# Optimization experiments

Hardware: AMD Instinct MI355X
Metric: run time of the kernel (lower is better)

## Reference

```python
import jax, jax.numpy as jnp
import numpy as np

HIDDEN = 768
HEADS = 12
HEAD_DIM = HIDDEN // HEADS


def setup_inputs() -> dict:
    key = jax.random.key(0)
    ks = jax.random.split(key, 6)
    B, N = 32, 577  # N = 1 CLS + 576 patches
    x = jax.random.normal(ks[0], (B, N, HIDDEN), dtype=jnp.float32)
    seg_bias = jax.random.uniform(ks[1], (B, N - 1), dtype=jnp.float32)
    w_qkv = jax.random.normal(ks[2], (HIDDEN, 3 * HIDDEN), dtype=jnp.float32) * 0.02
    b_qkv = jnp.zeros((3 * HIDDEN,), dtype=jnp.float32)
    w_proj = jax.random.normal(ks[3], (HIDDEN, HIDDEN), dtype=jnp.float32) * 0.02
    b_proj = jnp.zeros((HIDDEN,), dtype=jnp.float32)
    seg_scale = jnp.ones((), dtype=jnp.float32)
    return {"x": x, "seg_bias": seg_bias, "w_qkv": w_qkv, "b_qkv": b_qkv,
            "w_proj": w_proj, "b_proj": b_proj, "seg_scale": seg_scale}


def reference(x, seg_bias, w_qkv, b_qkv, w_proj, b_proj, seg_scale):
    B, N, _ = x.shape
    scale = HEAD_DIM ** -0.5
    qkv = x @ w_qkv + b_qkv                       # (B, N, 3*H*D)
    qkv = qkv.reshape(B, N, 3, HEADS, HEAD_DIM)
    q = qkv[:, :, 0].transpose(0, 2, 1, 3)        # (B, H, N, D)
    k = qkv[:, :, 1].transpose(0, 2, 1, 3)
    v = qkv[:, :, 2].transpose(0, 2, 1, 3)
    attn = jnp.einsum('bhqd,bhkd->bhqk', q, k) * scale  # (B, H, N, N)
    # additive seg bias on CLS-query row, patch keys only (cols 1:)
    bias = (seg_bias * seg_scale)[:, None, None, :]     # (B,1,1,N-1)
    attn = attn.at[:, :, 0:1, 1:].add(bias)
    attn = jax.nn.softmax(attn, axis=-1)
    out = jnp.einsum('bhqk,bhkd->bhqd', attn, v)        # (B, H, N, D)
    out = out.transpose(0, 2, 1, 3).reshape(B, N, HIDDEN)
    return out @ w_proj + b_proj
```

## Files before the change

### kernel.cpp

```cpp
#include <hip/hip_runtime.h>


typedef unsigned short bf16_t;
typedef __attribute__((ext_vector_type(8))) short short8;
typedef __attribute__((ext_vector_type(4))) short short4v;
typedef __attribute__((ext_vector_type(4))) float f32x4;

#define B_    32
#define N_    577
#define BN_   18464
#define HID_  768
#define NH_   12
#define HD_   64
#define QKVC_ 2304
#define NPAD_ 640
#define PB_LD 68

__device__ __forceinline__ bf16_t f2bf(float f) {
  union { float f; unsigned u; } x; x.f = f;
  unsigned r = x.u + 0x7fffu + ((x.u >> 16) & 1u);
  return (bf16_t)(r >> 16);
}

__device__ __forceinline__ unsigned cvt_pk_bf16(float a, float b) {
  unsigned r;
  asm("v_cvt_pk_bf16_f32 %0, %1, %2" : "=v"(r) : "v"(a), "v"(b));
  return r;
}

__global__ __launch_bounds__(256) void cast_kernel(const float* __restrict__ in,
                                                   bf16_t* __restrict__ out, int n4) {
  int i = blockIdx.x * 256 + threadIdx.x;
  if (i >= n4) return;
  float4 v = ((const float4*)in)[i];
  ushort4 o;
  o.x = f2bf(v.x); o.y = f2bf(v.y); o.z = f2bf(v.z); o.w = f2bf(v.w);
  ((ushort4*)out)[i] = o;
}

__global__ __launch_bounds__(256) void transpose_cast_kernel(const float* __restrict__ in,
                                                             bf16_t* __restrict__ out,
                                                             int R, int C) {
  __shared__ float tile[32][33];
  int c0 = blockIdx.x * 32, r0 = blockIdx.y * 32;
  int tx = threadIdx.x, ty = threadIdx.y;
  #pragma unroll
  for (int i = ty; i < 32; i += 8)
    tile[i][tx] = in[(size_t)(r0 + i) * C + c0 + tx];
  __syncthreads();
  #pragma unroll
  for (int i = ty; i < 32; i += 8)
    out[(size_t)(c0 + i) * R + r0 + tx] = f2bf(tile[tx][i]);
}

__device__ __forceinline__ void stage256(const bf16_t* __restrict__ A,
                                         const bf16_t* __restrict__ Bt,
                                         int M, int m0, int n0, int kt,
                                         bf16_t* as, bf16_t* bs, int tid) {
  #pragma unroll
  for (int it = 0; it < 4; ++it) {
    int gi = it * 512 + tid;
    int row = gi >> 3;
    int ch = (gi & 7) ^ (row & 7);
    int gm = m0 + row; if (gm >= M) gm = M - 1;
    __builtin_amdgcn_global_load_lds(
        (const __attribute__((address_space(1))) unsigned int*)(A + (size_t)gm * 768 + kt + ch * 8),
        (__attribute__((address_space(3))) unsigned int*)(as + gi * 8), 16, 0, 0);
    int gn = n0 + row;
    __builtin_amdgcn_global_load_lds(
        (const __attribute__((address_space(1))) unsigned int*)(Bt + (size_t)gn * 768 + kt + ch * 8),
        (__attribute__((address_space(3))) unsigned int*)(bs + gi * 8), 16, 0, 0);
  }
}

template <int OUT_BF16>
__global__ __launch_bounds__(512, 1) void gemm_bf16_kernel(
    const bf16_t* __restrict__ A,
    const bf16_t* __restrict__ Bt,
    const float* __restrict__ bias,
    void* __restrict__ Cout,
    int M, int Nc) {
  __shared__ __align__(16) bf16_t As[2][256 * 64];
  __shared__ __align__(16) bf16_t Bs[2][256 * 64];

  const int tid  = threadIdx.x;
  const int lane = tid & 63, w = tid >> 6;
  const int quad = lane >> 4, l16 = lane & 15;
  const int xsw = l16 & 7;

  const int Mb = (M + 255) >> 8;
  const int Nb = Nc >> 8;
  const int np_full = Mb >> 3;
  const int rem = Mb - np_full * 8;
  int bid = blockIdx.x;
  int m_blk, n_blk;
  int body = np_full * 8 * Nb;
  if (bid < body) {
    int p = bid / (8 * Nb), local = bid % (8 * Nb);
    m_blk = p * 8 + (local & 7);
    n_blk = local >> 3;
  } else {
    int t2 = bid - body;
    m_blk = np_full * 8 + t2 % rem;
    n_blk = t2 / rem;
  }
  const int m0 = m_blk * 256, n0 = n_blk * 256;
  const int wm = (w >> 2) * 128, wn = (w & 3) * 64;

  f32x4 acc[8][4];
  #pragma unroll
  for (int i = 0; i < 8; ++i)
    #pragma unroll
    for (int j = 0; j < 4; ++j)
      acc[i][j] = (f32x4){0.f, 0.f, 0.f, 0.f};

  stage256(A, Bt, M, m0, n0, 0,  &As[0][0], &Bs[0][0], tid);
  stage256(A, Bt, M, m0, n0, 64, &As[1][0], &Bs[1][0], tid);

  for (int t = 0; t < 12; ++t) {
    bf16_t* as = &As[t & 1][0];
    bf16_t* bs = &Bs[t & 1][0];

    if (t == 11) asm volatile("s_waitcnt vmcnt(0)" ::: "memory");
    else         asm volatile("s_waitcnt vmcnt(8)" ::: "memory");
    __builtin_amdgcn_sched_barrier(0);
    __builtin_amdgcn_s_barrier();
    __builtin_amdgcn_sched_barrier(0);

    #pragma unroll
    for (int ks = 0; ks < 2; ++ks) {
      const int c = (ks * 4 + quad) ^ xsw;
      short8 af[8], bfr[4];
      #pragma unroll
      for (int i = 0; i < 8; ++i)
        af[i] = *(const short8*)(as + (wm + i * 16 + l16) * 64 + c * 8);
      #pragma unroll
      for (int j = 0; j < 4; ++j)
        bfr[j] = *(const short8*)(bs + (wn + j * 16 + l16) * 64 + c * 8);
      __builtin_amdgcn_s_setprio(1);
      #pragma unroll
      for (int i = 0; i < 8; ++i)
        #pragma unroll
        for (int j = 0; j < 4; ++j)
          acc[i][j] = __builtin_amdgcn_mfma_f32_16x16x32_bf16(af[i], bfr[j], acc[i][j], 0, 0, 0);
      __builtin_amdgcn_s_setprio(0);
    }

    if (t < 10) {
      __builtin_amdgcn_sched_barrier(0);
      __builtin_amdgcn_s_barrier();
      __builtin_amdgcn_sched_barrier(0);
      stage256(A, Bt, M, m0, n0, (t + 2) * 64, as, bs, tid);
    }
  }

  #pragma unroll
  for (int i = 0; i < 8; ++i) {
    int mrow_base = m0 + wm + i * 16 + quad * 4;
    #pragma unroll
    for (int j = 0; j < 4; ++j) {
      int col = n0 + wn + j * 16 + l16;
      float bs_ = bias[col];
      #pragma unroll
      for (int r = 0; r < 4; ++r) {
        int row = mrow_base + r;
        if (row < M) {
          float v = acc[i][j][r] + bs_;
          if (OUT_BF16)
            ((bf16_t*)Cout)[(size_t)row * Nc + col] = f2bf(v);
          else
            ((float*)Cout)[(size_t)row * Nc + col] = v;
        }
      }
    }
  }
}

__global__ __launch_bounds__(256) void vt_kernel(const bf16_t* __restrict__ qkv,
                                                 bf16_t* __restrict__ vT) {
  const int t = blockIdx.x, h = blockIdx.y, b = blockIdx.z;
  const int tid = threadIdx.x;
  __shared__ bf16_t Ls[64 * 65];
  const int kv0 = t * 64;
  const bf16_t* Vp = qkv + (size_t)b * N_ * QKVC_ + 2 * HID_ + h * HD_;

  #pragma unroll
  for (int it = 0; it < 2; ++it) {
    int idx = it * 256 + tid;
    int row = idx >> 3, ch = idx & 7;
    int krow = kv0 + row; if (krow > N_ - 1) krow = N_ - 1;
    short8 v8 = *(const short8*)(Vp + (size_t)krow * QKVC_ + ch * 8);
    #pragma unroll
    for (int j = 0; j < 8; ++j)
      Ls[(ch * 8 + j) * 65 + row] = (bf16_t)v8[j];
  }
  __syncthreads();
  bf16_t* outp = vT + ((size_t)(b * NH_ + h) * HD_) * NPAD_;
  #pragma unroll
  for (int it = 0; it < 2; ++it) {
    int idx = it * 256 + tid;
    int d = idx >> 3, kc = idx & 7;
    short8 o8;
    #pragma unroll
    for (int j = 0; j < 8; ++j) {
      int p = kc * 8 + j;
      int ky = ((p & 3) << 4) | (p >> 2);
      o8[j] = (short)Ls[d * 65 + ky];
    }
    *(short8*)(outp + (size_t)d * NPAD_ + kv0 + kc * 8) = o8;
  }
}

template <int MI>
__device__ __forceinline__ void attn_body(
    int b, int h, int qbase,
    const bf16_t* __restrict__ qkv, const bf16_t* __restrict__ vT,
    const float* __restrict__ seg_bias, const float* __restrict__ seg_scale,
    bf16_t* __restrict__ out,
    bf16_t* Ks0, bf16_t* Ks1, bf16_t* Vt0, bf16_t* Vt1, bf16_t* PbAll) {
  const int tid = threadIdx.x;
  const int w = tid >> 6, lane = tid & 63;
  const int quad = lane >> 4, l16 = lane & 15;
  const int xsw = l16 & 7;

  const bf16_t* Qbase = qkv + (size_t)b * N_ * QKVC_ + h * HD_;
  const bf16_t* Kbase = Qbase + HID_;
  const bf16_t* Vtb   = vT + ((size_t)(b * NH_ + h) * HD_) * NPAD_;

  const float ssl = seg_scale[0] * 1.44269504f;

  {
    int row = tid >> 3;
    int ch = (tid & 7) ^ (row & 7);
    __builtin_amdgcn_global_load_lds(
        (const __attribute__((address_space(1))) unsigned int*)(Kbase + (size_t)row * QKVC_ + ch * 8),
        (__attribute__((address_space(3))) unsigned int*)(Ks0 + tid * 8), 16, 0, 0);
    __builtin_amdgcn_global_load_lds(
        (const __attribute__((address_space(1))) unsigned int*)(Vtb + (size_t)row * NPAD_ + ch * 8),
        (__attribute__((address_space(3))) unsigned int*)(Vt0 + tid * 8), 16, 0, 0);
  }

  const int q0 = qbase + w * (MI * 16);
  short8 qf[MI][2];
  #pragma unroll
  for (int mi = 0; mi < MI; ++mi) {
    int qr = q0 + mi * 16 + l16;
    if (qr > N_ - 1) qr = N_ - 1;
    qf[mi][0] = *(const short8*)(Qbase + (size_t)qr * QKVC_ + quad * 8);
    qf[mi][1] = *(const short8*)(Qbase + (size_t)qr * QKVC_ + 32 + quad * 8);
  }
  const float qsc = 0.125f * 1.44269504f;
  #pragma unroll
  for (int mi = 0; mi < MI; ++mi)
    #pragma unroll
    for (int c = 0; c < 2; ++c)
      #pragma unroll
      for (int j = 0; j < 8; ++j) {
        unsigned u = ((unsigned)(unsigned short)qf[mi][c][j]) << 16;
        union { unsigned u; float f; } x; x.u = u;
        qf[mi][c][j] = (short)f2bf(x.f * qsc);
      }

  const f32x4 z4 = {0.f, 0.f, 0.f, 0.f};
  f32x4 o[MI][4];
  f32x4 ls[MI];
  #pragma unroll
  for (int mi = 0; mi < MI; ++mi) {
    ls[mi] = z4;
    #pragma unroll
    for (int j = 0; j < 4; ++j) o[mi][j] = z4;
  }

  short8 ones;
  #pragma unroll
  for (int j = 0; j < 8; ++j) ones[j] = (short)0x3F80;

  const bool bias_wave = (qbase == 0 && w == 0);
  bf16_t* pw = PbAll + w * 16 * PB_LD;

  for (int t = 0; t < 9; ++t) {
    const int cur = t & 1;

    __builtin_amdgcn_s_barrier();
    __builtin_amdgcn_sched_barrier(0);

    {
      const int kv1 = (t + 1) * 64;
      bf16_t* ksn = cur ? Ks0 : Ks1;
      bf16_t* vtn = cur ? Vt0 : Vt1;
      int row = tid >> 3;
      int ch = (tid & 7) ^ (row & 7);
      int krow = kv1 + row; if (krow > N_ - 1) krow = N_ - 1;
      __builtin_amdgcn_global_load_lds(
          (const __attribute__((address_space(1))) unsigned int*)(Kbase + (size_t)krow * QKVC_ + ch * 8),
          (__attribute__((address_space(3))) unsigned int*)(ksn + tid * 8), 16, 0, 0);
      __builtin_amdgcn_global_load_lds(
          (const __attribute__((address_space(1))) unsigned int*)(Vtb + (size_t)row * NPAD_ + kv1 + ch * 8),
          (__attribute__((address_space(3))) unsigned int*)(vtn + tid * 8), 16, 0, 0);
    }

    asm volatile("s_waitcnt vmcnt(2)" ::: "memory");
    __builtin_amdgcn_sched_barrier(0);
    __builtin_amdgcn_s_barrier();
    __builtin_amdgcn_sched_barrier(0);

    const bf16_t* ks = cur ? Ks1 : Ks0;
    const bf16_t* vt = cur ? Vt1 : Vt0;

    f32x4 s[MI][4];
    __builtin_amdgcn_s_setprio(1);
    #pragma unroll
    for (int sub = 0; sub < 4; ++sub) {
      short8 k0 = *(const short8*)(ks + (sub * 16 + l16) * 64 + (quad ^ xsw) * 8);
      short8 k1 = *(const short8*)(ks + (sub * 16 + l16) * 64 + ((4 + quad) ^ xsw) * 8);
      #pragma unroll
      for (int mi = 0; mi < MI; ++mi) {
        s[mi][sub] = __builtin_amdgcn_mfma_f32_16x16x32_bf16(qf[mi][0], k0, z4, 0, 0, 0);
        s[mi][sub] = __builtin_amdgcn_mfma_f32_16x16x32_bf16(qf[mi][1], k1, s[mi][sub], 0, 0, 0);
      }
    }
    __builtin_amdgcn_s_setprio(0);

    if (bias_wave && quad == 0) {
      const int kv0 = t * 64;
      #pragma unroll
      for (int sub = 0; sub < 4; ++sub) {
        int key = kv0 + sub * 16 + l16;
        if (key >= 1)
          s[0][sub][0] += seg_bias[b * (N_ - 1) + key - 1] * ssl;
      }
    }

    #pragma unroll
    for (int mi = 0; mi < MI; ++mi) {
      #pragma unroll
      for (int r = 0; r < 4; ++r) {
        float p0 = __builtin_amdgcn_exp2f(s[mi][0][r]);
        float p1 = __builtin_amdgcn_exp2f(s[mi][1][r]);
        float p2 = __builtin_amdgcn_exp2f(s[mi][2][r]);
        float p3 = __builtin_amdgcn_exp2f(s[mi][3][r]);
        uint2 pk;
        pk.x = cvt_pk_bf16(p0, p1);
        pk.y = cvt_pk_bf16(p2, p3);
        *(uint2*)(pw + (quad * 4 + r) * PB_LD + l16 * 4) = pk;
      }

      const bf16_t* pr = pw + l16 * PB_LD + quad * 8;
      union { short8 v; short4v hv[2]; } pa0, pa1;
      pa0.hv[0] = *(const short4v*)(pr);
      pa0.hv[1] = *(const short4v*)(pr + 4);
      pa1.hv[0] = *(const short4v*)(pr + 32);
      pa1.hv[1] = *(const short4v*)(pr + 36);
      __builtin_amdgcn_s_setprio(1);
      ls[mi] = __builtin_amdgcn_mfma_f32_16x16x32_bf16(pa0.v, ones, ls[mi], 0, 0, 0);
      ls[mi] = __builtin_amdgcn_mfma_f32_16x16x32_bf16(pa1.v, ones, ls[mi], 0, 0, 0);
      #pragma unroll
      for (int ds = 0; ds < 4; ++ds) {
        short8 vb0 = *(const short8*)(vt + (ds * 16 + l16) * 64 + (quad ^ xsw) * 8);
        short8 vb1 = *(const short8*)(vt + (ds * 16 + l16) * 64 + ((4 + quad) ^ xsw) * 8);
        o[mi][ds] = __builtin_amdgcn_mfma_f32_16x16x32_bf16(pa0.v, vb0, o[mi][ds], 0, 0, 0);
        o[mi][ds] = __builtin_amdgcn_mfma_f32_16x16x32_bf16(pa1.v, vb1, o[mi][ds], 0, 0, 0);
      }
      __builtin_amdgcn_s_setprio(0);
    }
  }

  {
    asm volatile("s_waitcnt vmcnt(0)" ::: "memory");
    __builtin_amdgcn_sched_barrier(0);
    __builtin_amdgcn_s_barrier();
    __builtin_amdgcn_sched_barrier(0);

    const bf16_t* ks = Ks1;
    const bf16_t* vt = Vt1;

    short8 k0 = *(const short8*)(ks + l16 * 64 + (quad ^ xsw) * 8);
    short8 k1 = *(const short8*)(ks + l16 * 64 + ((4 + quad) ^ xsw) * 8);
    f32x4 s9[MI];
    #pragma unroll
    for (int mi = 0; mi < MI; ++mi) {
      s9[mi] = __builtin_amdgcn_mfma_f32_16x16x32_bf16(qf[mi][0], k0, z4, 0, 0, 0);
      s9[mi] = __builtin_amdgcn_mfma_f32_16x16x32_bf16(qf[mi][1], k1, s9[mi], 0, 0, 0);
    }
    if (bias_wave && quad == 0 && l16 == 0)
      s9[0][0] += seg_bias[b * (N_ - 1) + (N_ - 2)] * ssl;

    #pragma unroll
    for (int mi = 0; mi < MI; ++mi) {
      #pragma unroll
      for (int r = 0; r < 4; ++r) {
        float p0 = (l16 == 0) ? __builtin_amdgcn_exp2f(s9[mi][r]) : 0.f;
        uint2 pk;
        pk.x = cvt_pk_bf16(p0, 0.f);
        pk.y = 0u;
        *(uint2*)(pw + (quad * 4 + r) * PB_LD + l16 * 4) = pk;
      }
      const bf16_t* pr = pw + l16 * PB_LD + quad * 8;
      union { short8 v; short4v hv[2]; } pa0;
      pa0.hv[0] = *(const short4v*)(pr);
      pa0.hv[1] = *(const short4v*)(pr + 4);
      ls[mi] = __builtin_amdgcn_mfma_f32_16x16x32_bf16(pa0.v, ones, ls[mi], 0, 0, 0);
      #pragma unroll
      for (int ds = 0; ds < 4; ++ds) {
        short8 vb0 = *(const short8*)(vt + (ds * 16 + l16) * 64 + (quad ^ xsw) * 8);
        o[mi][ds] = __builtin_amdgcn_mfma_f32_16x16x32_bf16(pa0.v, vb0, o[mi][ds], 0, 0, 0);
      }
    }
  }

  #pragma unroll
  for (int mi = 0; mi < MI; ++mi)
    #pragma unroll
    for (int r = 0; r < 4; ++r) {
      float inv = 1.0f / ls[mi][r];
      int row = q0 + mi * 16 + quad * 4 + r;
      if (row < N_) {
        size_t base = ((size_t)b * N_ + row) * HID_ + h * HD_;
        #pragma unroll
        for (int ds = 0; ds < 4; ++ds)
          out[base + ds * 16 + l16] = f2bf(o[mi][ds][r] * inv);
      }
    }
}

__global__ __launch_bounds__(512) void attn_kernel(
    const bf16_t* __restrict__ qkv,
    const bf16_t* __restrict__ vT,
    const float* __restrict__ seg_bias,
    const float* __restrict__ seg_scale,
    bf16_t* __restrict__ out) {
  __shared__ __align__(16) bf16_t Ks[2][64 * 64];
  __shared__ __align__(16) bf16_t Vt[2][64 * 64];
  __shared__ __align__(16) bf16_t Pb[8][16 * PB_LD];

  const int bid = blockIdx.x;
  if (bid < 768) {
    const int pair = bid % 384, qblk = bid / 384;
    attn_body<2>(pair / NH_, pair % NH_, qblk * 256,
                 qkv, vT, seg_bias, seg_scale, out,
                 &Ks[0][0], &Ks[1][0], &Vt[0][0], &Vt[1][0], &Pb[0][0]);
  } else {
    const int pair = bid - 768;
    attn_body<1>(pair / NH_, pair % NH_, 512,
                 qkv, vT, seg_bias, seg_scale, out,
                 &Ks[0][0], &Ks[1][0], &Vt[0][0], &Vt[1][0], &Pb[0][0]);
  }
}

extern "C" void kernel_launch(void* const* d_in, const int* in_sizes, int n_in,
                              void* d_out, int out_size, void* d_ws, size_t ws_size,
                              hipStream_t stream) {
  const float* x         = (const float*)d_in[0];
  const float* seg_bias  = (const float*)d_in[1];
  const float* w_qkv     = (const float*)d_in[2];
  const float* b_qkv     = (const float*)d_in[3];
  const float* w_proj    = (const float*)d_in[4];
  const float* b_proj    = (const float*)d_in[5];
  const float* seg_scale = (const float*)d_in[6];

  char* ws = (char*)d_ws;
  bf16_t* xb     = (bf16_t*)ws;
  bf16_t* wqkvT  = (bf16_t*)(ws + 28360704);
  bf16_t* wprojT = (bf16_t*)(ws + 31899648);
  bf16_t* qkvb   = (bf16_t*)(ws + 33079296);
  bf16_t* vT     = (bf16_t*)(ws + 118161408);
  bf16_t* attnb  = xb;

  cast_kernel<<<(BN_ * HID_ / 4) / 256, 256, 0, stream>>>(x, xb, BN_ * HID_ / 4);
  dim3 tb(32, 8);
  transpose_cast_kernel<<<dim3(QKVC_ / 32, HID_ / 32), tb, 0, stream>>>(w_qkv, wqkvT, HID_, QKVC_);
  transpose_cast_kernel<<<dim3(HID_ / 32, HID_ / 32), tb, 0, stream>>>(w_proj, wprojT, HID_, HID_);

  gemm_bf16_kernel<1><<<73 * (QKVC_ / 256), 512, 0, stream>>>(
      xb, wqkvT, b_qkv, (void*)qkvb, BN_, QKVC_);

  vt_kernel<<<dim3(10, NH_, B_), 256, 0, stream>>>(qkvb, vT);

  attn_kernel<<<1152, 512, 0, stream>>>(qkvb, vT, seg_bias, seg_scale, attnb);

  gemm_bf16_kernel<0><<<73 * (HID_ / 256), 512, 0, stream>>>(
      attnb, wprojT, b_proj, d_out, BN_, HID_);
}
```

Baseline: 330.7 us.

## Interleave half-tile global-to-LDS loads with MFMA quadrants in GEMM main loop

```diff
diff --git a/kernel.cpp b/kernel.cpp
--- a/kernel.cpp
+++ b/kernel.cpp
@@ -28,6 +28,10 @@
   return r;
 }
 
+#define PHASE_BAR() do { __builtin_amdgcn_sched_barrier(0); \
+                         __builtin_amdgcn_s_barrier();      \
+                         __builtin_amdgcn_sched_barrier(0); } while (0)
+
 __global__ __launch_bounds__(256) void cast_kernel(const float* __restrict__ in,
                                                    bf16_t* __restrict__ out, int n4) {
   int i = blockIdx.x * 256 + threadIdx.x;
@@ -53,24 +57,55 @@
     out[(size_t)(c0 + i) * R + r0 + tx] = f2bf(tile[tx][i]);
 }
 
-__device__ __forceinline__ void stage256(const bf16_t* __restrict__ A,
-                                         const bf16_t* __restrict__ Bt,
-                                         int M, int m0, int n0, int kt,
-                                         bf16_t* as, bf16_t* bs, int tid) {
-  #pragma unroll
-  for (int it = 0; it < 4; ++it) {
+__device__ __forceinline__ void stage_half(const bf16_t* __restrict__ G,
+                                           int grow0, int gmax, int kt,
+                                           bf16_t* lds_half, int tid) {
+  #pragma unroll
+  for (int it = 0; it < 2; ++it) {
     int gi = it * 512 + tid;
     int row = gi >> 3;
     int ch = (gi & 7) ^ (row & 7);
-    int gm = m0 + row; if (gm >= M) gm = M - 1;
+    int gr = grow0 + row; if (gr >= gmax) gr = gmax - 1;
     __builtin_amdgcn_global_load_lds(
-        (const __attribute__((address_space(1))) unsigned int*)(A + (size_t)gm * 768 + kt + ch * 8),
-        (__attribute__((address_space(3))) unsigned int*)(as + gi * 8), 16, 0, 0);
-    int gn = n0 + row;
-    __builtin_amdgcn_global_load_lds(
-        (const __attribute__((address_space(1))) unsigned int*)(Bt + (size_t)gn * 768 + kt + ch * 8),
-        (__attribute__((address_space(3))) unsigned int*)(bs + gi * 8), 16, 0, 0);
-  }
+        (const __attribute__((address_space(1))) unsigned int*)(G + (size_t)gr * 768 + kt + ch * 8),
+        (__attribute__((address_space(3))) unsigned int*)(lds_half + gi * 8), 16, 0, 0);
+  }
+}
+
+__device__ __forceinline__ void ld_a4(short8 (&af)[4][2], const bf16_t* as,
+                                      int rbase, int l16, int quad, int xsw) {
+  #pragma unroll
+  for (int i = 0; i < 4; ++i) {
+    const bf16_t* p = as + (rbase + i * 16 + l16) * 64;
+    af[i][0] = *(const short8*)(p + (quad ^ xsw) * 8);
+    af[i][1] = *(const short8*)(p + ((4 + quad) ^ xsw) * 8);
+  }
+}
+
+__device__ __forceinline__ void ld_b2(short8 (&bfr)[2][2], const bf16_t* bs,
+                                      int rbase, int l16, int quad, int xsw) {
+  #pragma unroll
+  for (int j = 0; j < 2; ++j) {
+    const bf16_t* p = bs + (rbase + j * 16 + l16) * 64;
+    bfr[j][0] = *(const short8*)(p + (quad ^ xsw) * 8);
+    bfr[j][1] = *(const short8*)(p + ((4 + quad) ^ xsw) * 8);
+  }
+}
+
+template <int MH, int NH>
+__device__ __forceinline__ void mfma_quad(f32x4 (&acc)[8][4],
+                                          const short8 (&af)[4][2],
+                                          const short8 (&bfr)[2][2]) {
+  __builtin_amdgcn_s_setprio(1);
+  #pragma unroll
+  for (int ks = 0; ks < 2; ++ks)
+    #pragma unroll
+    for (int i = 0; i < 4; ++i)
+      #pragma unroll
+      for (int j = 0; j < 2; ++j)
+        acc[MH * 4 + i][NH * 2 + j] = __builtin_amdgcn_mfma_f32_16x16x32_bf16(
+            af[i][ks], bfr[j][ks], acc[MH * 4 + i][NH * 2 + j], 0, 0, 0);
+  __builtin_amdgcn_s_setprio(0);
 }
 
 template <int OUT_BF16>
@@ -114,44 +149,51 @@
     for (int j = 0; j < 4; ++j)
       acc[i][j] = (f32x4){0.f, 0.f, 0.f, 0.f};
 
-  stage256(A, Bt, M, m0, n0, 0,  &As[0][0], &Bs[0][0], tid);
-  stage256(A, Bt, M, m0, n0, 64, &As[1][0], &Bs[1][0], tid);
-
-  for (int t = 0; t < 12; ++t) {
-    bf16_t* as = &As[t & 1][0];
-    bf16_t* bs = &Bs[t & 1][0];
-
-    if (t == 11) asm volatile("s_waitcnt vmcnt(0)" ::: "memory");
-    else         asm volatile("s_waitcnt vmcnt(8)" ::: "memory");
-    __builtin_amdgcn_sched_barrier(0);
-    __builtin_amdgcn_s_barrier();
-    __builtin_amdgcn_sched_barrier(0);
-
-    #pragma unroll
-    for (int ks = 0; ks < 2; ++ks) {
-      const int c = (ks * 4 + quad) ^ xsw;
-      short8 af[8], bfr[4];
-      #pragma unroll
-      for (int i = 0; i < 8; ++i)
-        af[i] = *(const short8*)(as + (wm + i * 16 + l16) * 64 + c * 8);
-      #pragma unroll
-      for (int j = 0; j < 4; ++j)
-        bfr[j] = *(const short8*)(bs + (wn + j * 16 + l16) * 64 + c * 8);
-      __builtin_amdgcn_s_setprio(1);
-      #pragma unroll
-      for (int i = 0; i < 8; ++i)
-        #pragma unroll
-        for (int j = 0; j < 4; ++j)
-          acc[i][j] = __builtin_amdgcn_mfma_f32_16x16x32_bf16(af[i], bfr[j], acc[i][j], 0, 0, 0);
-      __builtin_amdgcn_s_setprio(0);
-    }
-
-    if (t < 10) {
-      __builtin_amdgcn_sched_barrier(0);
-      __builtin_amdgcn_s_barrier();
-      __builtin_amdgcn_sched_barrier(0);
-      stage256(A, Bt, M, m0, n0, (t + 2) * 64, as, bs, tid);
-    }
+  const int NK = 12;
+
+  stage_half(A,  m0,       M,  0,  &As[0][0],        tid);
+  stage_half(A,  m0 + 128, M,  0,  &As[0][0] + 8192, tid);
+  stage_half(Bt, n0,       Nc, 0,  &Bs[0][0],        tid);
+  stage_half(Bt, n0 + 128, Nc, 0,  &Bs[0][0] + 8192, tid);
+  stage_half(A,  m0,       M,  64, &As[1][0],        tid);
+  stage_half(A,  m0 + 128, M,  64, &As[1][0] + 8192, tid);
+  stage_half(Bt, n0,       Nc, 64, &Bs[1][0],        tid);
+  stage_half(Bt, n0 + 128, Nc, 64, &Bs[1][0] + 8192, tid);
+
+  for (int t = 0; t < NK; ++t) {
+    bf16_t* as  = &As[t & 1][0];
+    bf16_t* bs  = &Bs[t & 1][0];
+    bf16_t* asn = &As[(t + 1) & 1][0];
+    bf16_t* bsn = &Bs[(t + 1) & 1][0];
+    const int kt1 = (t + 1) * 64, kt2 = (t + 2) * 64;
+
+    if (t == 0)           asm volatile("s_waitcnt vmcnt(8)" ::: "memory");
+    else if (t == NK - 1) asm volatile("s_waitcnt vmcnt(0)" ::: "memory");
+    else                  asm volatile("s_waitcnt vmcnt(2)" ::: "memory");
+    PHASE_BAR();
+
+    short8 af[4][2], bfr[2][2];
+
+    ld_a4(af, as, wm, l16, quad, xsw);
+    ld_b2(bfr, bs, wn, l16, quad, xsw);
+    if (t >= 1 && t + 1 < NK) stage_half(A, m0 + 128, M, kt1, asn + 8192, tid);
+    mfma_quad<0, 0>(acc, af, bfr);
+    PHASE_BAR();
+
+    ld_b2(bfr, bs, wn + 32, l16, quad, xsw);
+    if (t >= 1 && t + 1 < NK) stage_half(Bt, n0, Nc, kt1, bsn, tid);
+    mfma_quad<0, 1>(acc, af, bfr);
+    PHASE_BAR();
+
+    ld_a4(af, as, wm + 64, l16, quad, xsw);
+    if (t >= 1 && t + 1 < NK) stage_half(Bt, n0 + 128, Nc, kt1, bsn + 8192, tid);
+    mfma_quad<1, 1>(acc, af, bfr);
+    PHASE_BAR();
+
+    ld_b2(bfr, bs, wn, l16, quad, xsw);
+    if (t + 2 < NK) stage_half(A, m0, M, kt2, as, tid);
+    mfma_quad<1, 0>(acc, af, bfr);
+    PHASE_BAR();
   }
 
   #pragma unroll
```

Measured after the change: 356.4 us. 1.08x slower.
